# Kernel optimization log

Measured on AMD Instinct MI355X. Metric: run time of the kernel, lower is better.

The kernel has to match this reference:

```python
import jax, jax.numpy as jnp
import numpy as np

KS = 3  # kernel_size


def _im2col(x):
    # x: (N, C, H, W) -> (N, H*W, C*KS*KS), matching torch unfold (channel-major,
    # kernel-position-minor) ordering with padding=1.
    N, C, H, W = x.shape
    xp = jnp.pad(x, ((0, 0), (0, 0), (1, 1), (1, 1)))
    patches = jnp.stack(
        [xp[:, :, i:i + H, j:j + W] for i in range(KS) for j in range(KS)],
        axis=2,
    )  # (N, C, 9, H, W)
    return patches.reshape(N, C * KS * KS, H * W).transpose(0, 2, 1)


def setup_inputs() -> dict:
    key = jax.random.key(0)
    k1, k2, k3, k4, k5 = jax.random.split(key, 5)
    N, C, H, W = 4, 64, 192, 192
    outC = 3
    return {
        "lr_features": jax.random.normal(k1, (N, C, H, W), dtype=jnp.float32),
        "W1": jax.random.normal(k2, (3, 256), dtype=jnp.float32) * 0.05,
        "b1": jax.random.normal(k3, (256,), dtype=jnp.float32) * 0.05,
        "W2": jax.random.normal(k4, (256, KS * KS * C * outC), dtype=jnp.float32) * 0.05,
        "b2": jax.random.normal(k5, (KS * KS * C * outC,), dtype=jnp.float32) * 0.05,
        "sr_scale": 4,
    }


def reference(lr_features, W1, b1, W2, b2, sr_scale):
    # Integer sr_scale: mask_mat is all-true and pos_mat_small is the s*s grid
    # of sub-pixel offsets [1/s, i/s, j/s] for i, j in [0, s).
    N, C, H, W = lr_features.shape
    s = int(np.ceil(sr_scale))
    inv = 1.0 / float(sr_scale)
    off = jnp.arange(s, dtype=jnp.float32) * inv
    pos = jnp.stack(jnp.meshgrid(off, off, indexing="ij"), axis=-1).reshape(s * s, 2)
    pos = jnp.concatenate(
        [jnp.full((s * s, 1), inv, dtype=jnp.float32), pos], axis=1
    )  # (s^2, 3)

    # Pos2Weight MLP -> per-subpixel dynamic conv weights (s^2, C*9, outC)
    hidden = jax.nn.relu(pos @ W1 + b1)
    local_weight = (hidden @ W2 + b2).reshape(s * s, KS * KS * C, -1)
    outC = local_weight.shape[-1]

    cols = _im2col(lr_features)  # (N, H*W, C*9)
    # batched small matmul: each sub-pixel position has its own filter
    out = jnp.einsum("npk,sko->nspo", cols, local_weight)  # (N, s^2, H*W, outC)
    out = out.reshape(N, s, s, H, W, outC)
    out = out.transpose(0, 5, 3, 1, 4, 2).reshape(N, outC, s * H, s * W)
    return out
```

## Files before the change

### kernel.cpp

```cpp
#include <hip/hip_runtime.h>


#define HH   192
#define WWD  192
#define SS   4
#define OC   3
#define PO   48
#define HID  256
#define W2LD 1728

typedef short  bf16x8 __attribute__((ext_vector_type(8)));
typedef float  f32x4  __attribute__((ext_vector_type(4)));

static __device__ __forceinline__ short f2bf(float f) {
    unsigned u = __float_as_uint(f);
    unsigned r = (u + 0x7fffu + ((u >> 16) & 1u)) >> 16;
    return (short)r;
}

static __device__ __forceinline__ void pin(bf16x8& v) {
    asm volatile("" : "+v"(v));
}

__global__ __launch_bounds__(256) void lw_kernel(
        const float* __restrict__ W1, const float* __restrict__ b1,
        const float* __restrict__ W2, const float* __restrict__ b2,
        short* __restrict__ lwb) {
    __shared__ float hlds[HID];
    const int tid = threadIdx.x;
    const int p   = blockIdx.y;
    {
        const float pi = (float)(p >> 2) * 0.25f;
        const float pj = (float)(p & 3) * 0.25f;
        const float v = 0.25f * W1[tid] + pi * W1[HID + tid] + pj * W1[2 * HID + tid]
                      + b1[tid];
        hlds[tid] = v > 0.f ? v : 0.f;
    }
    __syncthreads();

    const int col = blockIdx.x * 256 + tid;
    if (col < W2LD) {
        float a = 0.f;
#pragma unroll 32
        for (int h = 0; h < HID; ++h)
            a += hlds[h] * W2[h * W2LD + col];
        const int o = col % 3, kc = col / 3;
        const int tap = kc % 9, c = kc / 9;
        lwb[(tap * PO + p * 3 + o) * 64 + c] = f2bf(a + b2[col]);
    }
}

__global__ __launch_bounds__(192, 3) void meta_up_mfma(
        const float* __restrict__ x, const short* __restrict__ lwb,
        float* __restrict__ out) {
    __shared__ __align__(16) short smem[3 * 66 * 64];
    short* xlds = smem;
    float* obuf = (float*)smem;

    const int strip = (blockIdx.x & 7) * 288 + (blockIdx.x >> 3);
    const int n   = strip / (HH * 3);
    const int rem = strip % (HH * 3);
    const int h   = rem / 3;
    const int wch = rem % 3;
    const int w0  = wch * 64;

    const int tid  = threadIdx.x;
    const int lane = tid & 63, wv = tid >> 6;
    const int quad = lane >> 4, l15 = lane & 15;

    bf16x8 Bfrag[18];
#pragma unroll
    for (int tap = 0; tap < 9; ++tap)
#pragma unroll
        for (int kc2 = 0; kc2 < 2; ++kc2)
            Bfrag[tap * 2 + kc2] = *(const bf16x8*)
                &lwb[(tap * PO + wv * 16 + l15) * 64 + kc2 * 32 + quad * 8];
#pragma unroll
    for (int i = 0; i < 18; ++i) pin(Bfrag[i]);

    {
        const int gr  = h + wv - 1;
        const bool rok = (unsigned)gr < (unsigned)HH;
        const int gc  = w0 - 1 + lane;
        const bool cok = rok && ((unsigned)gc < (unsigned)WWD);
        const float* __restrict__ xr =
            x + ((size_t)n * 64 * HH + (size_t)(rok ? gr : 0)) * WWD + (cok ? gc : 0);
#pragma unroll
        for (int cb = 0; cb < 8; ++cb) {
            bf16x8 pk;
#pragma unroll
            for (int cc = 0; cc < 8; ++cc) {
                const float vv = cok ? xr[(size_t)(cb * 8 + cc) * HH * WWD] : 0.f;
                pk[cc] = f2bf(vv);
            }
            *(bf16x8*)&xlds[(wv * 66 + lane) * 64 + ((cb ^ (lane & 7)) << 3)] = pk;
        }
        if (lane < 16) {
            const int jt = 64 + (lane >> 3);
            const int cb = lane & 7;
            const int gc2 = w0 - 1 + jt;
            const bool cok2 = rok && ((unsigned)gc2 < (unsigned)WWD);
            bf16x8 pk;
#pragma unroll
            for (int cc = 0; cc < 8; ++cc) {
                const float vv = cok2 ?
                    x[((size_t)(n * 64 + cb * 8 + cc) * HH + gr) * WWD + gc2] : 0.f;
                pk[cc] = f2bf(vv);
            }
            *(bf16x8*)&xlds[(wv * 66 + jt) * 64 + ((cb ^ (jt & 7)) << 3)] = pk;
        }
    }
    __syncthreads();

    f32x4 acc[4];
#pragma unroll
    for (int mt = 0; mt < 4; ++mt) acc[mt] = (f32x4){0.f, 0.f, 0.f, 0.f};

#pragma unroll
    for (int tap = 0; tap < 9; ++tap) {
        const int di = tap / 3, dj = tap % 3;
#pragma unroll
        for (int kc2 = 0; kc2 < 2; ++kc2) {
            const bf16x8 b = Bfrag[tap * 2 + kc2];
#pragma unroll
            for (int mt = 0; mt < 4; ++mt) {
                const int col = mt * 16 + l15 + dj;
                const int blk = (kc2 * 4 + quad) ^ (col & 7);
                bf16x8 a = *(const bf16x8*)&xlds[(di * 66 + col) * 64 + (blk << 3)];
                acc[mt] = __builtin_amdgcn_mfma_f32_16x16x32_bf16(a, b, acc[mt], 0, 0, 0);
            }
        }
    }

    __syncthreads();
    {
        const int po = wv * 16 + l15;
        const int o  = po % 3;
        const int p  = po / 3;
        const int si = p >> 2, sj = p & 3;
        const int osi = o * 4 + si;
#pragma unroll
        for (int mt = 0; mt < 4; ++mt)
#pragma unroll
            for (int r4 = 0; r4 < 4; ++r4) {
                const int wl = mt * 16 + quad * 4 + r4;
                obuf[osi * 260 + wl * 4 + sj] = acc[mt][r4];
            }
    }
    __syncthreads();
    {
        const int osi = tid >> 4;
        const int c16 = tid & 15;
        const int o = osi >> 2, si = osi & 3;
        const size_t base =
            ((size_t)(n * OC + o) * (SS * HH) + (size_t)(SS * h + si)) * (SS * WWD)
            + (size_t)(4 * w0) + c16 * 16;
        const float* __restrict__ src = &obuf[osi * 260 + c16 * 16];
#pragma unroll
        for (int i = 0; i < 4; ++i)
            *(float4*)&out[base + i * 4] = *(const float4*)&src[i * 4];
    }
}

extern "C" void kernel_launch(void* const* d_in, const int* in_sizes, int n_in,
                              void* d_out, int out_size, void* d_ws, size_t ws_size,
                              hipStream_t stream) {
    const float* x  = (const float*)d_in[0];
    const float* W1 = (const float*)d_in[1];
    const float* b1 = (const float*)d_in[2];
    const float* W2 = (const float*)d_in[3];
    const float* b2 = (const float*)d_in[4];
    float* out = (float*)d_out;
    short* lwb = (short*)d_ws;

    lw_kernel<<<dim3(7, 16), 256, 0, stream>>>(W1, b1, W2, b2, lwb);
    meta_up_mfma<<<4 * HH * 3, 192, 0, stream>>>(x, lwb, out);
}
```

Measured before the change: 128.4 us.

## Pre-transpose input to channel-last bf16 in a merged prep kernel

Adds a prep pass that converts the NCHW fp32 input into an NHWC bf16 buffer in the workspace, fused into the same launch as the local-weight MLP kernel. The main MFMA kernel then loads 16-byte contiguous channel vectors per pixel instead of doing strided scalar fp32 loads across channels and converting them. This removes uncoalesced gathers and per-element conversion from the hot kernel, at the cost of an extra round trip of the input through global memory and a larger prep launch.

```diff
diff --git a/kernel.cpp b/kernel.cpp
--- a/kernel.cpp
+++ b/kernel.cpp
@@ -22,36 +22,64 @@
     asm volatile("" : "+v"(v));
 }
 
-__global__ __launch_bounds__(256) void lw_kernel(
+__global__ __launch_bounds__(256) void prep_kernel(
+        const float* __restrict__ x,
         const float* __restrict__ W1, const float* __restrict__ b1,
         const float* __restrict__ W2, const float* __restrict__ b2,
-        short* __restrict__ lwb) {
-    __shared__ float hlds[HID];
-    const int tid = threadIdx.x;
-    const int p   = blockIdx.y;
-    {
-        const float pi = (float)(p >> 2) * 0.25f;
-        const float pj = (float)(p & 3) * 0.25f;
-        const float v = 0.25f * W1[tid] + pi * W1[HID + tid] + pj * W1[2 * HID + tid]
-                      + b1[tid];
-        hlds[tid] = v > 0.f ? v : 0.f;
-    }
-    __syncthreads();
-
-    const int col = blockIdx.x * 256 + tid;
-    if (col < W2LD) {
-        float a = 0.f;
+        short* __restrict__ lwb, short* __restrict__ xt) {
+    const int b = blockIdx.x;
+    const int t = threadIdx.x;
+    if (b < 112) {
+        __shared__ float hlds[HID];
+        const int p = b / 7;
+        {
+            const float pi = (float)(p >> 2) * 0.25f;
+            const float pj = (float)(p & 3) * 0.25f;
+            const float v = 0.25f * W1[t] + pi * W1[HID + t] + pj * W1[2 * HID + t]
+                          + b1[t];
+            hlds[t] = v > 0.f ? v : 0.f;
+        }
+        __syncthreads();
+        const int col = (b % 7) * 256 + t;
+        if (col < W2LD) {
+            float a = 0.f;
 #pragma unroll 32
-        for (int h = 0; h < HID; ++h)
-            a += hlds[h] * W2[h * W2LD + col];
-        const int o = col % 3, kc = col / 3;
-        const int tap = kc % 9, c = kc / 9;
-        lwb[(tap * PO + p * 3 + o) * 64 + c] = f2bf(a + b2[col]);
+            for (int hh = 0; hh < HID; ++hh)
+                a += hlds[hh] * W2[hh * W2LD + col];
+            const int o = col % 3, kc = col / 3;
+            const int tap = kc % 9, c = kc / 9;
+            lwb[(tap * PO + p * 3 + o) * 64 + c] = f2bf(a + b2[col]);
+        }
+    } else {
+        __shared__ short tl[64][72];
+        const int bb = b - 112;
+        const int wt = bb % 3;
+        const int h  = (bb / 3) % HH;
+        const int n  = bb / (3 * HH);
+        const int w0 = wt * 64;
+#pragma unroll
+        for (int i = 0; i < 4; ++i) {
+            const int idx = i * 256 + t;
+            const int c   = idx >> 4;
+            const int j4  = idx & 15;
+            const float4 v = *(const float4*)
+                &x[(((size_t)(n * 64 + c)) * HH + h) * WWD + w0 + j4 * 4];
+            tl[j4 * 4 + 0][c] = f2bf(v.x);
+            tl[j4 * 4 + 1][c] = f2bf(v.y);
+            tl[j4 * 4 + 2][c] = f2bf(v.z);
+            tl[j4 * 4 + 3][c] = f2bf(v.w);
+        }
+        __syncthreads();
+        const int w  = t >> 2;
+        const int c0 = (t & 3) * 16;
+        short* dst = &xt[(((size_t)n * HH + h) * WWD + w0 + w) * 64 + c0];
+        *(bf16x8*)&dst[0] = *(const bf16x8*)&tl[w][c0];
+        *(bf16x8*)&dst[8] = *(const bf16x8*)&tl[w][c0 + 8];
     }
 }
 
 __global__ __launch_bounds__(192, 3) void meta_up_mfma(
-        const float* __restrict__ x, const short* __restrict__ lwb,
+        const short* __restrict__ xt, const short* __restrict__ lwb,
         float* __restrict__ out) {
     __shared__ __align__(16) short smem[3 * 66 * 64];
     short* xlds = smem;
@@ -81,33 +109,33 @@
     {
         const int gr  = h + wv - 1;
         const bool rok = (unsigned)gr < (unsigned)HH;
-        const int gc  = w0 - 1 + lane;
-        const bool cok = rok && ((unsigned)gc < (unsigned)WWD);
-        const float* __restrict__ xr =
-            x + ((size_t)n * 64 * HH + (size_t)(rok ? gr : 0)) * WWD + (cok ? gc : 0);
-#pragma unroll
-        for (int cb = 0; cb < 8; ++cb) {
-            bf16x8 pk;
-#pragma unroll
-            for (int cc = 0; cc < 8; ++cc) {
-                const float vv = cok ? xr[(size_t)(cb * 8 + cc) * HH * WWD] : 0.f;
-                pk[cc] = f2bf(vv);
-            }
-            *(bf16x8*)&xlds[(wv * 66 + lane) * 64 + ((cb ^ (lane & 7)) << 3)] = pk;
+        const short* __restrict__ src_row =
+            xt + (size_t)(n * HH + (rok ? gr : 0)) * (WWD * 64);
+        const bf16x8 z = {0, 0, 0, 0, 0, 0, 0, 0};
+        bf16x8 vv[8];
+#pragma unroll
+        for (int i = 0; i < 8; ++i) {
+            const int q  = i * 64 + lane;
+            const int j  = q >> 3, cb = q & 7;
+            const int gc = w0 - 1 + j;
+            const bool ok = rok && ((unsigned)gc < (unsigned)WWD);
+            vv[i] = ok ? *(const bf16x8*)&src_row[(size_t)(ok ? gc : 0) * 64 + cb * 8]
+                       : z;
+        }
+#pragma unroll
+        for (int i = 0; i < 8; ++i) {
+            const int q = i * 64 + lane;
+            const int j = q >> 3, cb = q & 7;
+            *(bf16x8*)&xlds[(wv * 66 + j) * 64 + ((cb ^ (j & 7)) << 3)] = vv[i];
         }
         if (lane < 16) {
-            const int jt = 64 + (lane >> 3);
-            const int cb = lane & 7;
-            const int gc2 = w0 - 1 + jt;
-            const bool cok2 = rok && ((unsigned)gc2 < (unsigned)WWD);
-            bf16x8 pk;
-#pragma unroll
-            for (int cc = 0; cc < 8; ++cc) {
-                const float vv = cok2 ?
-                    x[((size_t)(n * 64 + cb * 8 + cc) * HH + gr) * WWD + gc2] : 0.f;
-                pk[cc] = f2bf(vv);
-            }
-            *(bf16x8*)&xlds[(wv * 66 + jt) * 64 + ((cb ^ (jt & 7)) << 3)] = pk;
+            const int q  = 512 + lane;
+            const int j  = q >> 3, cb = q & 7;
+            const int gc = w0 - 1 + j;
+            const bool ok = rok && ((unsigned)gc < (unsigned)WWD);
+            const bf16x8 v = ok ?
+                *(const bf16x8*)&src_row[(size_t)(ok ? gc : 0) * 64 + cb * 8] : z;
+            *(bf16x8*)&xlds[(wv * 66 + j) * 64 + ((cb ^ (j & 7)) << 3)] = v;
         }
     }
     __syncthreads();
@@ -172,7 +200,8 @@
     const float* b2 = (const float*)d_in[4];
     float* out = (float*)d_out;
     short* lwb = (short*)d_ws;
-
-    lw_kernel<<<dim3(7, 16), 256, 0, stream>>>(W1, b1, W2, b2, lwb);
-    meta_up_mfma<<<4 * HH * 3, 192, 0, stream>>>(x, lwb, out);
-}
+    short* xt  = (short*)d_ws + 32768;
+
+    prep_kernel<<<112 + 4 * HH * 3, 256, 0, stream>>>(x, W1, b1, W2, b2, lwb, xt);
+    meta_up_mfma<<<4 * HH * 3, 192, 0, stream>>>(xt, lwb, out);
+}
```

Result: faster. 121.7 us (-5.2%).
